# Kernel optimization log

Measured on AMD Instinct MI355X. Metric: run time of the kernel, lower is better.

## Reference

```python
import jax, jax.numpy as jnp
import numpy as np

B, T, C, H = 8, 2048, 1024, 128


def setup_inputs() -> dict:
    key = jax.random.key(0)
    k1, k2, k3, k4 = jax.random.split(key, 4)
    x = jax.random.normal(k1, (B, T, C), dtype=jnp.float32)
    # Linear(n_embd, head_size, bias=False): weight is [head_size, n_embd] in torch,
    # applied as x @ W.T; we store W already transposed as [C, H].
    s = 1.0 / np.sqrt(C)
    Wk = jax.random.normal(k2, (C, H), dtype=jnp.float32) * s
    Wq = jax.random.normal(k3, (C, H), dtype=jnp.float32) * s
    Wv = jax.random.normal(k4, (C, H), dtype=jnp.float32) * s
    return {"x": x, "Wk": Wk, "Wq": Wq, "Wv": Wv}


def reference(x, Wk, Wq, Wv):
    # k, q, v projections
    k = jnp.einsum("btc,ch->bth", x, Wk)
    q = jnp.einsum("btc,ch->bth", x, Wq)
    v = jnp.einsum("btc,ch->bth", x, Wv)
    scale = k.shape[-1] ** -0.5
    wei = jnp.einsum("bqh,bkh->bqk", q, k) * scale  # [B,T,T]
    # causal mask: tril == 0 -> -inf
    Tq = x.shape[1]
    causal = jnp.tril(jnp.ones((Tq, Tq), dtype=bool))
    wei = jnp.where(causal, wei, -jnp.inf)
    wei = jax.nn.softmax(wei, axis=-1)
    # dropout p=0.0 -> identity
    out = jnp.einsum("bqk,bkh->bqh", wei, v)  # [B,T,H]
    return out
```

## Files before the change

kernel.cpp:

```cpp
#include <hip/hip_runtime.h>

typedef unsigned short u16;
typedef __attribute__((ext_vector_type(8))) short bf16x8;
typedef __attribute__((ext_vector_type(4))) float f32x4;
typedef __attribute__((ext_vector_type(4))) unsigned int u32x4;
typedef __attribute__((ext_vector_type(2))) unsigned int u32x2;

#define MFMA16(a, b, c) __builtin_amdgcn_mfma_f32_16x16x32_bf16((a), (b), (c), 0, 0, 0)

static constexpr int Bn = 8, Tn = 2048, Cn = 1024, Hn = 128;

static __device__ __forceinline__ u16 f2bf(float f) {
  union { float f; unsigned u; } v;
  v.f = f;
  unsigned r = v.u + 0x7fffu + ((v.u >> 16) & 1u);
  return (u16)(r >> 16);
}

static __device__ __forceinline__ float bf2f(u16 h) {
  union { unsigned u; float f; } v;
  v.u = ((unsigned)h) << 16;
  return v.f;
}

static __device__ __forceinline__ unsigned pack2(float a, float b) {
  return (unsigned)f2bf(a) | ((unsigned)f2bf(b) << 16);
}

__global__ __launch_bounds__(256) void wt_kernel(const float* __restrict__ Wk,
                                                 const float* __restrict__ Wq,
                                                 const float* __restrict__ Wv,
                                                 u16* __restrict__ Wt) {
  __shared__ u16 tile[64][65];
  const int c0 = blockIdx.x * 64;
  const int h0 = blockIdx.y * 64;
  const int z = blockIdx.z;
  const float* W = (z == 0) ? Wk : (z == 1) ? Wq : Wv;
  u16* dst = Wt + (size_t)z * Hn * Cn;
  const int tx = threadIdx.x & 63;
  const int ty = threadIdx.x >> 6;
#pragma unroll
  for (int i = 0; i < 16; ++i) {
    int r = ty * 16 + i;
    tile[r][tx] = f2bf(W[(size_t)(c0 + r) * Hn + h0 + tx]);
  }
  __syncthreads();
#pragma unroll
  for (int i = 0; i < 16; ++i) {
    int r = ty * 16 + i;
    dst[(size_t)(h0 + r) * Cn + c0 + tx] = tile[tx][r];
  }
}

__global__ __launch_bounds__(512, 4) void proj_kernel(const float* __restrict__ X,
                                                      const u16* __restrict__ Wt,
                                                      u16* __restrict__ Kb,
                                                      u16* __restrict__ Qb,
                                                      u16* __restrict__ Vt) {
  __shared__ u16 Xs[64][72];
  __shared__ u16 Ws[384][72];

  const int m0 = blockIdx.x * 64;
  const int tid = threadIdx.x;
  const int w = tid >> 6;
  const int wm = w & 1;
  const int wh = w >> 1;
  const int lane = tid & 63;
  const int l15 = lane & 15, lg = lane >> 4;

  const int xr = tid >> 3;
  const int xc = (tid & 7) * 8;
  const float* xptr = X + (size_t)(m0 + xr) * Cn + xc;
  const u16* wptr = Wt + (size_t)xr * Cn + xc;

  f32x4 acc[6][2] = {};
  f32x4 xl0, xl1;
  bf16x8 wl[6];

  xl0 = *reinterpret_cast<const f32x4*>(xptr);
  xl1 = *reinterpret_cast<const f32x4*>(xptr + 4);
#pragma unroll
  for (int i = 0; i < 6; ++i)
    wl[i] = *reinterpret_cast<const bf16x8*>(wptr + (size_t)i * 64 * Cn);

  for (int kt = 0; kt < Cn; kt += 64) {
    __syncthreads();
    {
      union { u16 h[8]; bf16x8 v; } cv;
#pragma unroll
      for (int j = 0; j < 4; ++j) {
        cv.h[j] = f2bf(xl0[j]);
        cv.h[4 + j] = f2bf(xl1[j]);
      }
      *reinterpret_cast<bf16x8*>(&Xs[xr][xc]) = cv.v;
#pragma unroll
      for (int i = 0; i < 6; ++i)
        *reinterpret_cast<bf16x8*>(&Ws[xr + i * 64][xc]) = wl[i];
    }
    if (kt + 64 < Cn) {
      xl0 = *reinterpret_cast<const f32x4*>(xptr + kt + 64);
      xl1 = *reinterpret_cast<const f32x4*>(xptr + kt + 64 + 4);
#pragma unroll
      for (int i = 0; i < 6; ++i)
        wl[i] = *reinterpret_cast<const bf16x8*>(wptr + (size_t)i * 64 * Cn + kt + 64);
    }
    __syncthreads();
#pragma unroll
    for (int kk = 0; kk < 2; ++kk) {
      const int ko = kk * 32 + lg * 8;
      bf16x8 af[6], bfx[2];
#pragma unroll
      for (int hf = 0; hf < 6; ++hf)
        af[hf] = *reinterpret_cast<const bf16x8*>(&Ws[wh * 96 + hf * 16 + l15][ko]);
#pragma unroll
      for (int mf = 0; mf < 2; ++mf)
        bfx[mf] = *reinterpret_cast<const bf16x8*>(&Xs[wm * 32 + mf * 16 + l15][ko]);
#pragma unroll
      for (int hf = 0; hf < 6; ++hf)
#pragma unroll
        for (int mf = 0; mf < 2; ++mf)
          acc[hf][mf] = MFMA16(af[hf], bfx[mf], acc[hf][mf]);
    }
  }

#pragma unroll
  for (int hf = 0; hf < 6; ++hf) {
    const int habs = wh * 96 + hf * 16 + lg * 4;
    const int p = habs >> 7;
    const int h = habs & 127;
    const float sc = (p == 1) ? 0.08838834764831845f : 1.0f;
#pragma unroll
    for (int mf = 0; mf < 2; ++mf) {
      const int m = m0 + wm * 32 + mf * 16 + l15;
      union { u16 h4[4]; u32x2 v; } pk;
#pragma unroll
      for (int r = 0; r < 4; ++r) pk.h4[r] = f2bf(acc[hf][mf][r] * sc);
      if (p == 0) {
        *reinterpret_cast<u32x2*>(&Kb[(size_t)m * Hn + h]) = pk.v;
      } else if (p == 1) {
        *reinterpret_cast<u32x2*>(&Qb[(size_t)m * Hn + h]) = pk.v;
      } else {
        const int b = m >> 11, t = m & (Tn - 1);
#pragma unroll
        for (int r = 0; r < 4; ++r)
          Vt[((size_t)b * Hn + h + r) * Tn + t] = pk.h4[r];
      }
    }
  }
}

__global__ __launch_bounds__(512) void attn_kernel(const u16* __restrict__ Qb,
                                                   const u16* __restrict__ Kb,
                                                   const u16* __restrict__ Vt,
                                                   float* __restrict__ Out) {
  __shared__ u16 Ks[128][136];
  __shared__ u16 Vs[128][136];
  __shared__ u16 Pl[8][16][72];
  __shared__ u16 Om[8][16][136];
  __shared__ float Ml[8][16][2];

  const int batch = blockIdx.x & 7;
  const int rrank = blockIdx.x >> 3;
  const int q0 = (31 - rrank) << 6;
  const int tid = threadIdx.x;
  const int w = tid >> 6;
  const int sw = w >> 1;
  const int par = w & 1;
  const int lane = tid & 63;
  const int l15 = lane & 15, lg = lane >> 4;

  const size_t bt = (size_t)batch * Tn;
  const int qrow = q0 + sw * 16;
  const int q = qrow + l15;

  bf16x8 qb[4];
#pragma unroll
  for (int kk = 0; kk < 4; ++kk)
    qb[kk] = *reinterpret_cast<const bf16x8*>(&Qb[(bt + q) * Hn + kk * 32 + lg * 8]);

  f32x4 o[8] = {};
  float m_r = -1e30f;
  float l_r = 0.f;

  const int nt = (q0 + 64 + 127) >> 7;

  u32x4 kreg[4], vreg[4];
#pragma unroll
  for (int i = 0; i < 4; ++i) {
    const int idx = tid + i * 512;
    const int row = idx >> 4, c8 = (idx & 15) * 8;
    kreg[i] = *reinterpret_cast<const u32x4*>(&Kb[(bt + row) * Hn + c8]);
    vreg[i] = *reinterpret_cast<const u32x4*>(&Vt[((size_t)batch * Hn + row) * Tn + c8]);
  }

  for (int t = 0; t < nt; ++t) {
    __syncthreads();
#pragma unroll
    for (int i = 0; i < 4; ++i) {
      const int idx = tid + i * 512;
      const int row = idx >> 4, c8 = (idx & 15) * 8;
      *reinterpret_cast<u32x4*>(&Ks[row][c8]) = kreg[i];
      *reinterpret_cast<u32x4*>(&Vs[row][c8]) = vreg[i];
    }
    __syncthreads();
    const int k0 = t << 7;
    if (t + 1 < nt) {
      const int kn = (t + 1) << 7;
#pragma unroll
      for (int i = 0; i < 4; ++i) {
        const int idx = tid + i * 512;
        const int row = idx >> 4, c8 = (idx & 15) * 8;
        kreg[i] = *reinterpret_cast<const u32x4*>(&Kb[(bt + kn + row) * Hn + c8]);
        vreg[i] = *reinterpret_cast<const u32x4*>(&Vt[((size_t)batch * Hn + row) * Tn + kn + c8]);
      }
    }

    const int kbase = k0 + par * 64;
    if (kbase <= qrow) {
      f32x4 s[4] = {};
#pragma unroll
      for (int nf = 0; nf < 4; ++nf) {
#pragma unroll
        for (int kk = 0; kk < 4; ++kk) {
          bf16x8 ka = *reinterpret_cast<const bf16x8*>(
              &Ks[par * 64 + nf * 16 + l15][kk * 32 + lg * 8]);
          s[nf] = MFMA16(ka, qb[kk], s[nf]);
        }
      }

      if (kbase + 63 > qrow) {
#pragma unroll
        for (int nf = 0; nf < 4; ++nf)
#pragma unroll
          for (int r = 0; r < 4; ++r)
            if (kbase + nf * 16 + lg * 4 + r > q) s[nf][r] = -1e30f;
      }

      float mx = -1e30f;
#pragma unroll
      for (int nf = 0; nf < 4; ++nf)
#pragma unroll
        for (int r = 0; r < 4; ++r) mx = fmaxf(mx, s[nf][r]);
      mx = fmaxf(mx, __shfl_xor(mx, 16));
      mx = fmaxf(mx, __shfl_xor(mx, 32));
      const float mn = fmaxf(m_r, mx);
      const float sc = __expf(m_r - mn);
      float rs = 0.f;
#pragma unroll
      for (int nf = 0; nf < 4; ++nf)
#pragma unroll
        for (int r = 0; r < 4; ++r) {
          s[nf][r] = __expf(s[nf][r] - mn);
          rs += s[nf][r];
        }
      rs += __shfl_xor(rs, 16);
      rs += __shfl_xor(rs, 32);
      l_r = l_r * sc + rs;
      m_r = mn;
#pragma unroll
      for (int n = 0; n < 8; ++n) o[n] *= sc;

#pragma unroll
      for (int nf = 0; nf < 4; ++nf) {
        u32x2 pv;
        pv.x = pack2(s[nf][0], s[nf][1]);
        pv.y = pack2(s[nf][2], s[nf][3]);
        *reinterpret_cast<u32x2*>(&Pl[w][l15][nf * 16 + lg * 4]) = pv;
      }
      asm volatile("s_waitcnt lgkmcnt(0)" ::: "memory");
      __builtin_amdgcn_sched_barrier(0);
      bf16x8 pb[2];
#pragma unroll
      for (int ks = 0; ks < 2; ++ks)
        pb[ks] = *reinterpret_cast<const bf16x8*>(&Pl[w][l15][ks * 32 + lg * 8]);

#pragma unroll
      for (int n = 0; n < 8; ++n) {
#pragma unroll
        for (int ks = 0; ks < 2; ++ks) {
          bf16x8 va = *reinterpret_cast<const bf16x8*>(
              &Vs[n * 16 + l15][par * 64 + ks * 32 + lg * 8]);
          o[n] = MFMA16(va, pb[ks], o[n]);
        }
      }
    }
  }

#pragma unroll
  for (int n = 0; n < 8; ++n) {
    u32x2 ov;
    ov.x = pack2(o[n][0], o[n][1]);
    ov.y = pack2(o[n][2], o[n][3]);
    *reinterpret_cast<u32x2*>(&Om[w][l15][n * 16 + lg * 4]) = ov;
  }
  if (lg == 0) {
    Ml[w][l15][0] = m_r;
    Ml[w][l15][1] = l_r;
  }
  __syncthreads();

  {
    const int row = tid >> 3;
    const int h0 = (tid & 7) * 16;
    const int s_ = row >> 4;
    const int r16 = row & 15;
    const int w0 = s_ * 2, w1 = w0 + 1;
    const float m0v = Ml[w0][r16][0], l0v = Ml[w0][r16][1];
    const float m1v = Ml[w1][r16][0], l1v = Ml[w1][r16][1];
    const float M = fmaxf(m0v, m1v);
    const float e0 = __expf(m0v - M), e1 = __expf(m1v - M);
    const float inv = 1.0f / (l0v * e0 + l1v * e1);
    u32x4 a0 = *reinterpret_cast<const u32x4*>(&Om[w0][r16][h0]);
    u32x4 a1 = *reinterpret_cast<const u32x4*>(&Om[w0][r16][h0 + 8]);
    u32x4 b0 = *reinterpret_cast<const u32x4*>(&Om[w1][r16][h0]);
    u32x4 b1 = *reinterpret_cast<const u32x4*>(&Om[w1][r16][h0 + 8]);
    float outv[16];
#pragma unroll
    for (int j = 0; j < 4; ++j) {
      outv[2 * j]     = (e0 * bf2f((u16)(a0[j] & 0xffffu)) + e1 * bf2f((u16)(b0[j] & 0xffffu))) * inv;
      outv[2 * j + 1] = (e0 * bf2f((u16)(a0[j] >> 16))     + e1 * bf2f((u16)(b0[j] >> 16))) * inv;
      outv[8 + 2 * j]     = (e0 * bf2f((u16)(a1[j] & 0xffffu)) + e1 * bf2f((u16)(b1[j] & 0xffffu))) * inv;
      outv[8 + 2 * j + 1] = (e0 * bf2f((u16)(a1[j] >> 16))     + e1 * bf2f((u16)(b1[j] >> 16))) * inv;
    }
    float* op = &Out[(bt + q0 + row) * Hn + h0];
#pragma unroll
    for (int j = 0; j < 4; ++j)
      *reinterpret_cast<f32x4*>(op + j * 4) = *reinterpret_cast<const f32x4*>(&outv[j * 4]);
  }
}

extern "C" void kernel_launch(void* const* d_in, const int* in_sizes, int n_in,
                              void* d_out, int out_size, void* d_ws, size_t ws_size,
                              hipStream_t stream) {
  const float* X = (const float*)d_in[0];
  const float* Wk = (const float*)d_in[1];
  const float* Wq = (const float*)d_in[2];
  const float* Wv = (const float*)d_in[3];

  char* ws = (char*)d_ws;
  u16* Wt = (u16*)(ws);
  u16* Kb = (u16*)(ws + 786432);
  u16* Qb = (u16*)(ws + 786432 + 4194304);
  u16* Vt = (u16*)(ws + 786432 + 2 * 4194304);
  float* Out = (float*)d_out;

  wt_kernel<<<dim3(16, 2, 3), 256, 0, stream>>>(Wk, Wq, Wv, Wt);
  proj_kernel<<<dim3(256), 512, 0, stream>>>(X, Wt, Kb, Qb, Vt);
  attn_kernel<<<dim3(Bn * 32), 512, 0, stream>>>(Qb, Kb, Vt, Out);
}
```

Baseline: 74.62 us.

## Split attention into 32-row query tiles with 4-way key split and direct V reads

Halves the query tile to 32 rows per block, doubling the grid to 512 blocks, and splits each 128-key tile four ways across warps instead of two. V is no longer staged in shared memory; MFMA operands are read straight from global/L2. K staging uses an XOR swizzle instead of padding, and all shared buffers are aliased into one array to cut LDS use. The final merge combines four partial softmax states per row. The aim is better occupancy and load balance, at the cost of more global V traffic and K reloads across the extra blocks.

```diff
diff --git a/kernel.cpp b/kernel.cpp
--- a/kernel.cpp
+++ b/kernel.cpp
@@ -153,21 +153,20 @@
                                                    const u16* __restrict__ Kb,
                                                    const u16* __restrict__ Vt,
                                                    float* __restrict__ Out) {
-  __shared__ u16 Ks[128][136];
-  __shared__ u16 Vs[128][136];
-  __shared__ u16 Pl[8][16][72];
-  __shared__ u16 Om[8][16][136];
+  __shared__ u16 SM[21504];
   __shared__ float Ml[8][16][2];
 
   const int batch = blockIdx.x & 7;
-  const int rrank = blockIdx.x >> 3;
-  const int q0 = (31 - rrank) << 6;
+  const int idx6 = blockIdx.x >> 3;
+  const int s32 = (idx6 < 32) ? (63 - idx6) : (idx6 - 32);
+  const int q0 = s32 << 5;
   const int tid = threadIdx.x;
   const int w = tid >> 6;
-  const int sw = w >> 1;
-  const int par = w & 1;
+  const int sw = w >> 2;
+  const int par = w & 3;
   const int lane = tid & 63;
   const int l15 = lane & 15, lg = lane >> 4;
+  const int swz = l15 & 7;
 
   const size_t bt = (size_t)batch * Tn;
   const int qrow = q0 + sw * 16;
@@ -182,72 +181,64 @@
   float m_r = -1e30f;
   float l_r = 0.f;
 
-  const int nt = (q0 + 64 + 127) >> 7;
-
-  u32x4 kreg[4], vreg[4];
-#pragma unroll
-  for (int i = 0; i < 4; ++i) {
-    const int idx = tid + i * 512;
-    const int row = idx >> 4, c8 = (idx & 15) * 8;
-    kreg[i] = *reinterpret_cast<const u32x4*>(&Kb[(bt + row) * Hn + c8]);
-    vreg[i] = *reinterpret_cast<const u32x4*>(&Vt[((size_t)batch * Hn + row) * Tn + c8]);
-  }
+  const int nt = (q0 + 32 + 127) >> 7;
+
+  u32x4 kreg[4];
+#define AK_LOAD(KN)                                                            \
+  _Pragma("unroll")                                                            \
+  for (int i = 0; i < 4; ++i) {                                                \
+    const int idx = tid + i * 512;                                             \
+    const int row = idx >> 4, c = idx & 15;                                    \
+    kreg[i] = *reinterpret_cast<const u32x4*>(&Kb[(bt + (KN) + row) * Hn + c * 8]); \
+  }
+
+#define AK_STAGE()                                                             \
+  _Pragma("unroll")                                                            \
+  for (int i = 0; i < 4; ++i) {                                                \
+    const int idx = tid + i * 512;                                             \
+    const int row = idx >> 4, c = idx & 15;                                    \
+    *reinterpret_cast<u32x4*>(&SM[row * 128 + ((c ^ (row & 7)) << 3)]) = kreg[i]; \
+  }
+
+  AK_LOAD(0)
 
   for (int t = 0; t < nt; ++t) {
     __syncthreads();
-#pragma unroll
-    for (int i = 0; i < 4; ++i) {
-      const int idx = tid + i * 512;
-      const int row = idx >> 4, c8 = (idx & 15) * 8;
-      *reinterpret_cast<u32x4*>(&Ks[row][c8]) = kreg[i];
-      *reinterpret_cast<u32x4*>(&Vs[row][c8]) = vreg[i];
-    }
+    AK_STAGE()
+    if (t + 1 < nt) AK_LOAD((t + 1) << 7)
     __syncthreads();
     const int k0 = t << 7;
-    if (t + 1 < nt) {
-      const int kn = (t + 1) << 7;
-#pragma unroll
-      for (int i = 0; i < 4; ++i) {
-        const int idx = tid + i * 512;
-        const int row = idx >> 4, c8 = (idx & 15) * 8;
-        kreg[i] = *reinterpret_cast<const u32x4*>(&Kb[(bt + kn + row) * Hn + c8]);
-        vreg[i] = *reinterpret_cast<const u32x4*>(&Vt[((size_t)batch * Hn + row) * Tn + kn + c8]);
-      }
-    }
-
-    const int kbase = k0 + par * 64;
+    const int kbase = k0 + par * 32;
     if (kbase <= qrow) {
-      f32x4 s[4] = {};
-#pragma unroll
-      for (int nf = 0; nf < 4; ++nf) {
+      f32x4 s[2] = {};
+#pragma unroll
+      for (int nf = 0; nf < 2; ++nf) {
+        const int krow = par * 32 + nf * 16 + l15;
 #pragma unroll
         for (int kk = 0; kk < 4; ++kk) {
           bf16x8 ka = *reinterpret_cast<const bf16x8*>(
-              &Ks[par * 64 + nf * 16 + l15][kk * 32 + lg * 8]);
+              &SM[krow * 128 + (((kk * 4 + lg) ^ swz) << 3)]);
           s[nf] = MFMA16(ka, qb[kk], s[nf]);
         }
       }
 
-      if (kbase + 63 > qrow) {
-#pragma unroll
-        for (int nf = 0; nf < 4; ++nf)
+      if (kbase + 31 > qrow) {
+#pragma unroll
+        for (int nf = 0; nf < 2; ++nf)
 #pragma unroll
           for (int r = 0; r < 4; ++r)
             if (kbase + nf * 16 + lg * 4 + r > q) s[nf][r] = -1e30f;
       }
 
-      float mx = -1e30f;
-#pragma unroll
-      for (int nf = 0; nf < 4; ++nf)
-#pragma unroll
-        for (int r = 0; r < 4; ++r) mx = fmaxf(mx, s[nf][r]);
+      float mx = fmaxf(fmaxf(fmaxf(s[0][0], s[0][1]), fmaxf(s[0][2], s[0][3])),
+                       fmaxf(fmaxf(s[1][0], s[1][1]), fmaxf(s[1][2], s[1][3])));
       mx = fmaxf(mx, __shfl_xor(mx, 16));
       mx = fmaxf(mx, __shfl_xor(mx, 32));
       const float mn = fmaxf(m_r, mx);
-      const float sc = __expf(m_r - mn);
+      const float scv = __expf(m_r - mn);
       float rs = 0.f;
 #pragma unroll
-      for (int nf = 0; nf < 4; ++nf)
+      for (int nf = 0; nf < 2; ++nf)
 #pragma unroll
         for (int r = 0; r < 4; ++r) {
           s[nf][r] = __expf(s[nf][r] - mn);
@@ -255,43 +246,40 @@
         }
       rs += __shfl_xor(rs, 16);
       rs += __shfl_xor(rs, 32);
-      l_r = l_r * sc + rs;
+      l_r = l_r * scv + rs;
       m_r = mn;
 #pragma unroll
-      for (int n = 0; n < 8; ++n) o[n] *= sc;
-
-#pragma unroll
-      for (int nf = 0; nf < 4; ++nf) {
+      for (int n = 0; n < 8; ++n) o[n] *= scv;
+
+      u16* PlW = &SM[16384 + w * 640 + l15 * 40];
+#pragma unroll
+      for (int nf = 0; nf < 2; ++nf) {
         u32x2 pv;
         pv.x = pack2(s[nf][0], s[nf][1]);
         pv.y = pack2(s[nf][2], s[nf][3]);
-        *reinterpret_cast<u32x2*>(&Pl[w][l15][nf * 16 + lg * 4]) = pv;
+        *reinterpret_cast<u32x2*>(&PlW[nf * 16 + lg * 4]) = pv;
       }
       asm volatile("s_waitcnt lgkmcnt(0)" ::: "memory");
       __builtin_amdgcn_sched_barrier(0);
-      bf16x8 pb[2];
-#pragma unroll
-      for (int ks = 0; ks < 2; ++ks)
-        pb[ks] = *reinterpret_cast<const bf16x8*>(&Pl[w][l15][ks * 32 + lg * 8]);
+      bf16x8 pb = *reinterpret_cast<const bf16x8*>(&PlW[lg * 8]);
 
 #pragma unroll
       for (int n = 0; n < 8; ++n) {
-#pragma unroll
-        for (int ks = 0; ks < 2; ++ks) {
-          bf16x8 va = *reinterpret_cast<const bf16x8*>(
-              &Vs[n * 16 + l15][par * 64 + ks * 32 + lg * 8]);
-          o[n] = MFMA16(va, pb[ks], o[n]);
-        }
-      }
-    }
-  }
+        bf16x8 va = *reinterpret_cast<const bf16x8*>(
+            &Vt[((size_t)batch * Hn + n * 16 + l15) * Tn + kbase + lg * 8]);
+        o[n] = MFMA16(va, pb, o[n]);
+      }
+    }
+  }
+
+  __syncthreads();
 
 #pragma unroll
   for (int n = 0; n < 8; ++n) {
     u32x2 ov;
     ov.x = pack2(o[n][0], o[n][1]);
     ov.y = pack2(o[n][2], o[n][3]);
-    *reinterpret_cast<u32x2*>(&Om[w][l15][n * 16 + lg * 4]) = ov;
+    *reinterpret_cast<u32x2*>(&SM[w * 2176 + l15 * 136 + n * 16 + lg * 4]) = ov;
   }
   if (lg == 0) {
     Ml[w][l15][0] = m_r;
@@ -300,32 +288,41 @@
   __syncthreads();
 
   {
-    const int row = tid >> 3;
-    const int h0 = (tid & 7) * 16;
-    const int s_ = row >> 4;
+    const int row = tid >> 4;
+    const int hc = tid & 15;
+    const int sw2 = row >> 4;
     const int r16 = row & 15;
-    const int w0 = s_ * 2, w1 = w0 + 1;
-    const float m0v = Ml[w0][r16][0], l0v = Ml[w0][r16][1];
-    const float m1v = Ml[w1][r16][0], l1v = Ml[w1][r16][1];
-    const float M = fmaxf(m0v, m1v);
-    const float e0 = __expf(m0v - M), e1 = __expf(m1v - M);
-    const float inv = 1.0f / (l0v * e0 + l1v * e1);
-    u32x4 a0 = *reinterpret_cast<const u32x4*>(&Om[w0][r16][h0]);
-    u32x4 a1 = *reinterpret_cast<const u32x4*>(&Om[w0][r16][h0 + 8]);
-    u32x4 b0 = *reinterpret_cast<const u32x4*>(&Om[w1][r16][h0]);
-    u32x4 b1 = *reinterpret_cast<const u32x4*>(&Om[w1][r16][h0 + 8]);
-    float outv[16];
-#pragma unroll
-    for (int j = 0; j < 4; ++j) {
-      outv[2 * j]     = (e0 * bf2f((u16)(a0[j] & 0xffffu)) + e1 * bf2f((u16)(b0[j] & 0xffffu))) * inv;
-      outv[2 * j + 1] = (e0 * bf2f((u16)(a0[j] >> 16))     + e1 * bf2f((u16)(b0[j] >> 16))) * inv;
-      outv[8 + 2 * j]     = (e0 * bf2f((u16)(a1[j] & 0xffffu)) + e1 * bf2f((u16)(b1[j] & 0xffffu))) * inv;
-      outv[8 + 2 * j + 1] = (e0 * bf2f((u16)(a1[j] >> 16))     + e1 * bf2f((u16)(b1[j] >> 16))) * inv;
-    }
-    float* op = &Out[(bt + q0 + row) * Hn + h0];
-#pragma unroll
-    for (int j = 0; j < 4; ++j)
-      *reinterpret_cast<f32x4*>(op + j * 4) = *reinterpret_cast<const f32x4*>(&outv[j * 4]);
+    const int wb = sw2 * 4;
+    float mw[4], lw[4];
+    float M = -1e30f;
+#pragma unroll
+    for (int i = 0; i < 4; ++i) {
+      mw[i] = Ml[wb + i][r16][0];
+      lw[i] = Ml[wb + i][r16][1];
+      M = fmaxf(M, mw[i]);
+    }
+    float e[4], L = 0.f;
+#pragma unroll
+    for (int i = 0; i < 4; ++i) {
+      e[i] = __expf(mw[i] - M);
+      L += lw[i] * e[i];
+    }
+    const float inv = 1.0f / L;
+    float outv[8] = {};
+#pragma unroll
+    for (int i = 0; i < 4; ++i) {
+      u32x4 ov = *reinterpret_cast<const u32x4*>(&SM[(wb + i) * 2176 + r16 * 136 + hc * 8]);
+#pragma unroll
+      for (int j = 0; j < 4; ++j) {
+        outv[2 * j] += e[i] * bf2f((u16)(ov[j] & 0xffffu));
+        outv[2 * j + 1] += e[i] * bf2f((u16)(ov[j] >> 16));
+      }
+    }
+#pragma unroll
+    for (int j = 0; j < 8; ++j) outv[j] *= inv;
+    float* op = &Out[(bt + q0 + row) * Hn + hc * 8];
+    *reinterpret_cast<f32x4*>(op) = *reinterpret_cast<const f32x4*>(&outv[0]);
+    *reinterpret_cast<f32x4*>(op + 4) = *reinterpret_cast<const f32x4*>(&outv[4]);
   }
 }
 
@@ -346,5 +343,5 @@
 
   wt_kernel<<<dim3(16, 2, 3), 256, 0, stream>>>(Wk, Wq, Wv, Wt);
   proj_kernel<<<dim3(256), 512, 0, stream>>>(X, Wt, Kb, Qb, Vt);
-  attn_kernel<<<dim3(Bn * 32), 512, 0, stream>>>(Qb, Kb, Vt, Out);
-}
+  attn_kernel<<<dim3(512), 512, 0, stream>>>(Qb, Kb, Vt, Out);
+}
```

After: 86.58 us. 16.0% more time.

## Double-buffer K/V tiles in LDS to drop one barrier per iteration

Applied to the files above, without the earlier changes.

Replaces the single K/V shared-memory buffers with two ping-pong buffers in one unified LDS array, which also aliases the output-merge scratch onto the K buffer area. Each iteration now computes on the current buffer, then stages the prefetched registers into the other buffer and issues the global load for two tiles ahead, so only one __syncthreads per iteration is needed. This is meant to overlap LDS staging and global loads with the MFMA work and to cut barrier stalls. The cost is roughly 158KB of LDS, which limits occupancy to one block per CU.

```diff
diff --git a/kernel.cpp b/kernel.cpp
--- a/kernel.cpp
+++ b/kernel.cpp
@@ -153,10 +153,7 @@
                                                    const u16* __restrict__ Kb,
                                                    const u16* __restrict__ Vt,
                                                    float* __restrict__ Out) {
-  __shared__ u16 Ks[128][136];
-  __shared__ u16 Vs[128][136];
-  __shared__ u16 Pl[8][16][72];
-  __shared__ u16 Om[8][16][136];
+  __shared__ u16 SM[78848];
   __shared__ float Ml[8][16][2];
 
   const int batch = blockIdx.x & 7;
@@ -185,45 +182,44 @@
   const int nt = (q0 + 64 + 127) >> 7;
 
   u32x4 kreg[4], vreg[4];
-#pragma unroll
-  for (int i = 0; i < 4; ++i) {
-    const int idx = tid + i * 512;
-    const int row = idx >> 4, c8 = (idx & 15) * 8;
-    kreg[i] = *reinterpret_cast<const u32x4*>(&Kb[(bt + row) * Hn + c8]);
-    vreg[i] = *reinterpret_cast<const u32x4*>(&Vt[((size_t)batch * Hn + row) * Tn + c8]);
-  }
+#define ATTN_LOAD(KN)                                                          \
+  _Pragma("unroll")                                                            \
+  for (int i = 0; i < 4; ++i) {                                                \
+    const int idx = tid + i * 512;                                             \
+    const int row = idx >> 4, c8 = (idx & 15) * 8;                             \
+    kreg[i] = *reinterpret_cast<const u32x4*>(&Kb[(bt + (KN) + row) * Hn + c8]); \
+    vreg[i] = *reinterpret_cast<const u32x4*>(                                 \
+        &Vt[((size_t)batch * Hn + row) * Tn + (KN) + c8]);                     \
+  }
+
+#define ATTN_STAGE(BUF)                                                        \
+  _Pragma("unroll")                                                            \
+  for (int i = 0; i < 4; ++i) {                                                \
+    const int idx = tid + i * 512;                                             \
+    const int row = idx >> 4, c8 = (idx & 15) * 8;                             \
+    *reinterpret_cast<u32x4*>(&SM[(BUF) * 34816 + row * 136 + c8]) = kreg[i];  \
+    *reinterpret_cast<u32x4*>(&SM[(BUF) * 34816 + 17408 + row * 136 + c8]) = vreg[i]; \
+  }
+
+  ATTN_LOAD(0)
+  ATTN_STAGE(0)
+  if (nt > 1) ATTN_LOAD(128)
+  __syncthreads();
 
   for (int t = 0; t < nt; ++t) {
-    __syncthreads();
-#pragma unroll
-    for (int i = 0; i < 4; ++i) {
-      const int idx = tid + i * 512;
-      const int row = idx >> 4, c8 = (idx & 15) * 8;
-      *reinterpret_cast<u32x4*>(&Ks[row][c8]) = kreg[i];
-      *reinterpret_cast<u32x4*>(&Vs[row][c8]) = vreg[i];
-    }
-    __syncthreads();
+    const int cur = t & 1;
     const int k0 = t << 7;
-    if (t + 1 < nt) {
-      const int kn = (t + 1) << 7;
-#pragma unroll
-      for (int i = 0; i < 4; ++i) {
-        const int idx = tid + i * 512;
-        const int row = idx >> 4, c8 = (idx & 15) * 8;
-        kreg[i] = *reinterpret_cast<const u32x4*>(&Kb[(bt + kn + row) * Hn + c8]);
-        vreg[i] = *reinterpret_cast<const u32x4*>(&Vt[((size_t)batch * Hn + row) * Tn + kn + c8]);
-      }
-    }
-
     const int kbase = k0 + par * 64;
     if (kbase <= qrow) {
+      const u16* KsB = &SM[cur * 34816];
+      const u16* VsB = &SM[cur * 34816 + 17408];
       f32x4 s[4] = {};
 #pragma unroll
       for (int nf = 0; nf < 4; ++nf) {
 #pragma unroll
         for (int kk = 0; kk < 4; ++kk) {
           bf16x8 ka = *reinterpret_cast<const bf16x8*>(
-              &Ks[par * 64 + nf * 16 + l15][kk * 32 + lg * 8]);
+              &KsB[(par * 64 + nf * 16 + l15) * 136 + kk * 32 + lg * 8]);
           s[nf] = MFMA16(ka, qb[kk], s[nf]);
         }
       }
@@ -244,7 +240,7 @@
       mx = fmaxf(mx, __shfl_xor(mx, 16));
       mx = fmaxf(mx, __shfl_xor(mx, 32));
       const float mn = fmaxf(m_r, mx);
-      const float sc = __expf(m_r - mn);
+      const float scv = __expf(m_r - mn);
       float rs = 0.f;
 #pragma unroll
       for (int nf = 0; nf < 4; ++nf)
@@ -255,35 +251,42 @@
         }
       rs += __shfl_xor(rs, 16);
       rs += __shfl_xor(rs, 32);
-      l_r = l_r * sc + rs;
+      l_r = l_r * scv + rs;
       m_r = mn;
 #pragma unroll
-      for (int n = 0; n < 8; ++n) o[n] *= sc;
-
+      for (int n = 0; n < 8; ++n) o[n] *= scv;
+
+      u16* PlW = &SM[69632 + w * 1152];
 #pragma unroll
       for (int nf = 0; nf < 4; ++nf) {
         u32x2 pv;
         pv.x = pack2(s[nf][0], s[nf][1]);
         pv.y = pack2(s[nf][2], s[nf][3]);
-        *reinterpret_cast<u32x2*>(&Pl[w][l15][nf * 16 + lg * 4]) = pv;
+        *reinterpret_cast<u32x2*>(&PlW[l15 * 72 + nf * 16 + lg * 4]) = pv;
       }
       asm volatile("s_waitcnt lgkmcnt(0)" ::: "memory");
       __builtin_amdgcn_sched_barrier(0);
       bf16x8 pb[2];
 #pragma unroll
       for (int ks = 0; ks < 2; ++ks)
-        pb[ks] = *reinterpret_cast<const bf16x8*>(&Pl[w][l15][ks * 32 + lg * 8]);
+        pb[ks] = *reinterpret_cast<const bf16x8*>(&PlW[l15 * 72 + ks * 32 + lg * 8]);
 
 #pragma unroll
       for (int n = 0; n < 8; ++n) {
 #pragma unroll
         for (int ks = 0; ks < 2; ++ks) {
           bf16x8 va = *reinterpret_cast<const bf16x8*>(
-              &Vs[n * 16 + l15][par * 64 + ks * 32 + lg * 8]);
+              &VsB[(n * 16 + l15) * 136 + par * 64 + ks * 32 + lg * 8]);
           o[n] = MFMA16(va, pb[ks], o[n]);
         }
       }
     }
+
+    if (t + 1 < nt) {
+      ATTN_STAGE(cur ^ 1)
+      if (t + 2 < nt) ATTN_LOAD((t + 2) << 7)
+    }
+    __syncthreads();
   }
 
 #pragma unroll
@@ -291,7 +294,7 @@
     u32x2 ov;
     ov.x = pack2(o[n][0], o[n][1]);
     ov.y = pack2(o[n][2], o[n][3]);
-    *reinterpret_cast<u32x2*>(&Om[w][l15][n * 16 + lg * 4]) = ov;
+    *reinterpret_cast<u32x2*>(&SM[w * 2176 + l15 * 136 + n * 16 + lg * 4]) = ov;
   }
   if (lg == 0) {
     Ml[w][l15][0] = m_r;
@@ -310,10 +313,12 @@
     const float M = fmaxf(m0v, m1v);
     const float e0 = __expf(m0v - M), e1 = __expf(m1v - M);
     const float inv = 1.0f / (l0v * e0 + l1v * e1);
-    u32x4 a0 = *reinterpret_cast<const u32x4*>(&Om[w0][r16][h0]);
-    u32x4 a1 = *reinterpret_cast<const u32x4*>(&Om[w0][r16][h0 + 8]);
-    u32x4 b0 = *reinterpret_cast<const u32x4*>(&Om[w1][r16][h0]);
-    u32x4 b1 = *reinterpret_cast<const u32x4*>(&Om[w1][r16][h0 + 8]);
+    const u16* Oa = &SM[w0 * 2176 + r16 * 136 + h0];
+    const u16* Ob = &SM[w1 * 2176 + r16 * 136 + h0];
+    u32x4 a0 = *reinterpret_cast<const u32x4*>(Oa);
+    u32x4 a1 = *reinterpret_cast<const u32x4*>(Oa + 8);
+    u32x4 b0 = *reinterpret_cast<const u32x4*>(Ob);
+    u32x4 b1 = *reinterpret_cast<const u32x4*>(Ob + 8);
     float outv[16];
 #pragma unroll
     for (int j = 0; j < 4; ++j) {
```

Result: no change. 73.37 us (-1.7%).
